# Performance work log

Hardware: AMD Instinct MI355X
Metric: run time of the kernel (lower is better)

Reference implementation:

```python
import jax, jax.numpy as jnp
import numpy as np

B, IN_CHAN, CHAN, H, W = 8, 64, 64, 56, 56


def setup_inputs() -> dict:
    key = jax.random.key(0)
    k1, k2, k3, k4 = jax.random.split(key, 4)
    x = jax.random.normal(k1, (B, IN_CHAN, H, W), dtype=jnp.float32)
    eye23 = jnp.eye(3, dtype=jnp.float32)[:2]  # [2,3] identity affine
    geoParams = eye23[None, None] + 0.1 * jax.random.normal(k2, (CHAN, IN_CHAN, 2, 3), dtype=jnp.float32)
    linComb = jax.random.uniform(k3, (CHAN, IN_CHAN), dtype=jnp.float32)
    boxParams = eye23[None] + 0.1 * jax.random.normal(k4, (CHAN, 2, 3), dtype=jnp.float32)
    return {"x": x, "geoParams": geoParams, "linComb": linComb, "boxParams": boxParams}


def _sample_coords(theta, Hs, Ws):
    # F.affine_grid with align_corners=False: base grid at pixel centers in [-1,1]
    xs = 2.0 * (jnp.arange(Ws, dtype=jnp.float32) + 0.5) / Ws - 1.0  # [W]
    ys = 2.0 * (jnp.arange(Hs, dtype=jnp.float32) + 0.5) / Hs - 1.0  # [H]
    gx = theta[..., 0, 0, None, None] * xs[None, :] + theta[..., 0, 1, None, None] * ys[:, None] + theta[..., 0, 2, None, None]
    gy = theta[..., 1, 0, None, None] * xs[None, :] + theta[..., 1, 1, None, None] * ys[:, None] + theta[..., 1, 2, None, None]
    # grid_sample unnormalize (align_corners=False)
    ix = ((gx + 1.0) * Ws - 1.0) / 2.0
    iy = ((gy + 1.0) * Hs - 1.0) / 2.0
    return ix, iy  # theta.shape[:-2] + (Hs, Ws)


def _corners(ix, iy, Hs, Ws):
    # bilinear corner flat-indices and weights (zero padding via validity mask)
    ix0 = jnp.floor(ix)
    iy0 = jnp.floor(iy)
    out = []
    for dx in (0.0, 1.0):
        for dy in (0.0, 1.0):
            cx = ix0 + dx
            cy = iy0 + dy
            w = (1.0 - jnp.abs(ix - cx)) * (1.0 - jnp.abs(iy - cy))
            valid = (cx >= 0) & (cx <= Ws - 1) & (cy >= 0) & (cy <= Hs - 1)
            idx = jnp.clip(cy, 0, Hs - 1).astype(jnp.int32) * Ws + jnp.clip(cx, 0, Ws - 1).astype(jnp.int32)
            out.append((idx, w * valid.astype(w.dtype)))
    return out


def reference(x, geoParams, linComb, boxParams):
    Bn, IC, Hs, Ws = x.shape
    C = geoParams.shape[0]
    HW = Hs * Ws
    ix, iy = _sample_coords(geoParams, Hs, Ws)  # [C, IC, H, W]
    flat = x.reshape(Bn, IC, HW)
    ic_idx = jnp.arange(IC)[None, :, None]  # broadcast with [C, IC, HW] indices
    out = jnp.zeros((Bn, C, HW), dtype=x.dtype)
    for idx, w in _corners(ix, iy, Hs, Ws):
        idxf = idx.reshape(C, IC, HW)
        wf = w.reshape(C, IC, HW)
        g = flat[:, ic_idx, idxf]  # [B, C, IC, HW] gathered corner values
        out = out + jnp.einsum('bcip,cip,ci->bcp', g, wf, linComb)
    out = out.reshape(Bn, C, Hs, Ws)
    # BoxPool: grid_sample of an all-ones image == sum of valid corner weights
    bix, biy = _sample_coords(boxParams, Hs, Ws)  # [C, H, W]
    box = jnp.zeros((C, Hs, Ws), dtype=x.dtype)
    for _, w in _corners(bix, biy, Hs, Ws):
        box = box + w
    return out * box[None]
```

## Files before the change

### kernel.cpp

```cpp
#include <hip/hip_runtime.h>

#define NB 8
#define ICN 64
#define NC 64
#define H 56
#define W 56
#define HW (H*W)
#define PH 58
#define PW 58
#define PHW (PH*PW)

typedef __attribute__((ext_vector_type(8))) _Float16 half8;

__global__ __launch_bounds__(256) void prep_kernel(
    const float* __restrict__ geo, const float* __restrict__ lin,
    float* __restrict__ prm)
{
    const int i = blockIdx.x * 256 + threadIdx.x;
    if (i >= NC * ICN) return;
    const float t00 = geo[i*6+0], t01 = geo[i*6+1], t02 = geo[i*6+2];
    const float t10 = geo[i*6+3], t11 = geo[i*6+4], t12 = geo[i*6+5];
    prm[i*8+0] = t00;
    prm[i*8+1] = t01;
    prm[i*8+2] = -27.5f*(t00+t01) + 28.f*t02 + 27.5f;
    prm[i*8+3] = t10;
    prm[i*8+4] = t11;
    prm[i*8+5] = -27.5f*(t10+t11) + 28.f*t12 + 27.5f;
    prm[i*8+6] = lin[i];
    prm[i*8+7] = 0.f;
}

__global__ __launch_bounds__(256) void transpose_pad_kernel(
    const float* __restrict__ x, _Float16* __restrict__ xt)
{
    const int id = blockIdx.x * 256 + threadIdx.x;
    if (id >= ICN * HW) return;
    const int ic = id / HW;
    const int p  = id - ic * HW;
    const int h  = p / W;
    const int w  = p - h * W;
    half8 v;
    #pragma unroll
    for (int b = 0; b < NB; ++b)
        v[b] = (_Float16)x[(size_t)b * ICN * HW + id];
    const size_t dst = ((size_t)ic * PHW + (size_t)(h + 1) * PW + (w + 1)) * NB;
    *(half8*)(xt + dst) = v;
}

__global__ __launch_bounds__(64) void geom_h_kernel(
    const _Float16* __restrict__ xt,
    const float* __restrict__ prm,
    const float* __restrict__ boxp,
    float* __restrict__ out)
{
    const int c = blockIdx.x;
    const int p = blockIdx.y * 64 + threadIdx.x;
    const int h = p / W;
    const int w = p - h * W;
    const float wf = (float)w, hf = (float)h;

    float acc[NB];
    #pragma unroll
    for (int b = 0; b < NB; ++b) acc[b] = 0.f;

    const float* pp = prm + (size_t)c * ICN * 8;

    for (int icc = 0; icc < ICN; icc += 4) {
        half8 hacc;
        #pragma unroll
        for (int b = 0; b < NB; ++b) hacc[b] = (_Float16)0.f;

        #pragma unroll
        for (int k = 0; k < 4; ++k) {
            const float* q = pp + (icc + k) * 8;
            const float ixf = fmaf(q[0], wf, fmaf(q[1], hf, q[2]));
            const float iyf = fmaf(q[3], wf, fmaf(q[4], hf, q[5]));
            const float l   = q[6];

            const float fcx0 = fminf(fmaxf(floorf(ixf), -1.f), 55.f);
            const float fcy0 = fminf(fmaxf(floorf(iyf), -1.f), 55.f);
            const float wx0 = fmaxf(0.f, 1.f - fabsf(ixf - fcx0));
            const float wx1 = fmaxf(0.f, 1.f - fabsf(ixf - fcx0 - 1.f));
            const float wy0 = fmaxf(0.f, 1.f - fabsf(iyf - fcy0));
            const float wy1 = fmaxf(0.f, 1.f - fabsf(iyf - fcy0 - 1.f));
            const float wy0l = wy0 * l, wy1l = wy1 * l;

            const _Float16 hw00 = (_Float16)(wx0 * wy0l);
            const _Float16 hw10 = (_Float16)(wx1 * wy0l);
            const _Float16 hw01 = (_Float16)(wx0 * wy1l);
            const _Float16 hw11 = (_Float16)(wx1 * wy1l);

            const int i00 = ((int)fcy0) * PW + (int)fcx0 + (PW + 1);
            const _Float16* base = xt + ((size_t)(icc + k) * PHW + i00) * NB;

            const half8 v00 = *(const half8*)(base);
            const half8 v10 = *(const half8*)(base + NB);
            const half8 v01 = *(const half8*)(base + PW * NB);
            const half8 v11 = *(const half8*)(base + (PW + 1) * NB);

            hacc += v00 * hw00 + v10 * hw10 + v01 * hw01 + v11 * hw11;
        }

        #pragma unroll
        for (int b = 0; b < NB; ++b) acc[b] += (float)hacc[b];
    }

    float box;
    {
        const float* bp = boxp + c*6;
        const float xs = 2.0f * (wf + 0.5f) / (float)W - 1.0f;
        const float ys = 2.0f * (hf + 0.5f) / (float)H - 1.0f;
        const float gx = bp[0]*xs + bp[1]*ys + bp[2];
        const float gy = bp[3]*xs + bp[4]*ys + bp[5];
        const float ixf = ((gx + 1.f)*(float)W - 1.f) * 0.5f;
        const float iyf = ((gy + 1.f)*(float)H - 1.f) * 0.5f;
        const float ix0 = floorf(ixf), iy0 = floorf(iyf);
        const float fx = ixf - ix0, fy = iyf - iy0;
        const int cx0 = (int)ix0, cy0 = (int)iy0;
        const int cx1 = cx0 + 1,  cy1 = cy0 + 1;
        const bool vx0 = (cx0 >= 0) && (cx0 < W);
        const bool vx1 = (cx1 >= 0) && (cx1 < W);
        const bool vy0 = (cy0 >= 0) && (cy0 < H);
        const bool vy1 = (cy1 >= 0) && (cy1 < H);
        box = (1.f-fx)*(1.f-fy)*((vx0 && vy0) ? 1.f : 0.f)
            + (1.f-fx)*fy     *((vx0 && vy1) ? 1.f : 0.f)
            + fx*(1.f-fy)     *((vx1 && vy0) ? 1.f : 0.f)
            + fx*fy           *((vx1 && vy1) ? 1.f : 0.f);
    }

    #pragma unroll
    for (int b = 0; b < NB; ++b)
        out[((size_t)b*NC + c)*HW + p] = acc[b] * box;
}

__global__ __launch_bounds__(256) void geom_kernel(
    const float* __restrict__ x, const float* __restrict__ geo,
    const float* __restrict__ lin, const float* __restrict__ boxp,
    float* __restrict__ out)
{
    const int c = blockIdx.x;
    const int p = blockIdx.y * blockDim.x + threadIdx.x;
    if (p >= HW) return;
    const int h = p / W;
    const int w = p - h * W;
    const float xs = 2.0f * ((float)w + 0.5f) / (float)W - 1.0f;
    const float ys = 2.0f * ((float)h + 0.5f) / (float)H - 1.0f;

    float acc[NB];
    #pragma unroll
    for (int b = 0; b < NB; ++b) acc[b] = 0.f;

    const float* gp = geo + c * ICN * 6;
    const float* lc = lin + c * ICN;

    for (int ic = 0; ic < ICN; ++ic) {
        const float t00 = gp[ic*6+0], t01 = gp[ic*6+1], t02 = gp[ic*6+2];
        const float t10 = gp[ic*6+3], t11 = gp[ic*6+4], t12 = gp[ic*6+5];
        const float l = lc[ic];
        const float gx = t00*xs + t01*ys + t02;
        const float gy = t10*xs + t11*ys + t12;
        const float ixf = ((gx + 1.f)*(float)W - 1.f) * 0.5f;
        const float iyf = ((gy + 1.f)*(float)H - 1.f) * 0.5f;
        const float ix0 = floorf(ixf), iy0 = floorf(iyf);
        const float fx = ixf - ix0, fy = iyf - iy0;
        const int cx0 = (int)ix0, cy0 = (int)iy0;
        const int cx1 = cx0 + 1,  cy1 = cy0 + 1;
        const bool vx0 = (cx0 >= 0) && (cx0 <= W-1);
        const bool vx1 = (cx1 >= 0) && (cx1 <= W-1);
        const bool vy0 = (cy0 >= 0) && (cy0 <= H-1);
        const bool vy1 = (cy1 >= 0) && (cy1 <= H-1);
        const float wx0 = 1.f - fx, wx1 = fx;
        const float wy0 = 1.f - fy, wy1 = fy;
        const float w00 = wx0*wy0 * ((vx0 && vy0) ? l : 0.f);
        const float w01 = wx0*wy1 * ((vx0 && vy1) ? l : 0.f);
        const float w10 = wx1*wy0 * ((vx1 && vy0) ? l : 0.f);
        const float w11 = wx1*wy1 * ((vx1 && vy1) ? l : 0.f);
        const int icx0 = min(max(cx0, 0), W-1);
        const int icx1 = min(max(cx1, 0), W-1);
        const int icy0 = min(max(cy0, 0), H-1);
        const int icy1 = min(max(cy1, 0), H-1);
        const int i00 = icy0*W + icx0;
        const int i01 = icy1*W + icx0;
        const int i10 = icy0*W + icx1;
        const int i11 = icy1*W + icx1;
        const float* xp = x + ic * HW;
        #pragma unroll
        for (int b = 0; b < NB; ++b) {
            const float* xb = xp + (size_t)b * ICN * HW;
            acc[b] += w00*xb[i00] + w01*xb[i01] + w10*xb[i10] + w11*xb[i11];
        }
    }

    float box;
    {
        const float* bp = boxp + c*6;
        const float gx = bp[0]*xs + bp[1]*ys + bp[2];
        const float gy = bp[3]*xs + bp[4]*ys + bp[5];
        const float ixf = ((gx + 1.f)*(float)W - 1.f) * 0.5f;
        const float iyf = ((gy + 1.f)*(float)H - 1.f) * 0.5f;
        const float ix0 = floorf(ixf), iy0 = floorf(iyf);
        const float fx = ixf - ix0, fy = iyf - iy0;
        const int cx0 = (int)ix0, cy0 = (int)iy0;
        const int cx1 = cx0 + 1,  cy1 = cy0 + 1;
        const bool vx0 = (cx0 >= 0) && (cx0 < W);
        const bool vx1 = (cx1 >= 0) && (cx1 < W);
        const bool vy0 = (cy0 >= 0) && (cy0 < H);
        const bool vy1 = (cy1 >= 0) && (cy1 < H);
        box = (1.f-fx)*(1.f-fy)*((vx0 && vy0) ? 1.f : 0.f)
            + (1.f-fx)*fy     *((vx0 && vy1) ? 1.f : 0.f)
            + fx*(1.f-fy)     *((vx1 && vy0) ? 1.f : 0.f)
            + fx*fy           *((vx1 && vy1) ? 1.f : 0.f);
    }
    #pragma unroll
    for (int b = 0; b < NB; ++b)
        out[((size_t)b*NC + c)*HW + p] = acc[b] * box;
}

extern "C" void kernel_launch(void* const* d_in, const int* in_sizes, int n_in,
                              void* d_out, int out_size, void* d_ws, size_t ws_size,
                              hipStream_t stream) {
    const float* x    = (const float*)d_in[0];
    const float* geo  = (const float*)d_in[1];
    const float* lin  = (const float*)d_in[2];
    const float* boxp = (const float*)d_in[3];
    float* out = (float*)d_out;

    const size_t xt_bytes  = (size_t)ICN * PHW * NB * sizeof(_Float16);
    const size_t prm_off   = (xt_bytes + 255) & ~(size_t)255;
    const size_t prm_bytes = (size_t)NC * ICN * 8 * sizeof(float);
    if (ws_size >= prm_off + prm_bytes) {
        _Float16* xt = (_Float16*)d_ws;
        float* prm = (float*)((char*)d_ws + prm_off);
        hipMemsetAsync(d_ws, 0, xt_bytes, stream);
        hipLaunchKernelGGL(prep_kernel, dim3((NC*ICN + 255)/256), dim3(256),
                           0, stream, geo, lin, prm);
        hipLaunchKernelGGL(transpose_pad_kernel, dim3((ICN*HW + 255)/256), dim3(256),
                           0, stream, x, xt);
        hipLaunchKernelGGL(geom_h_kernel, dim3(NC, 49), dim3(64),
                           0, stream, xt, prm, boxp, out);
    } else {
        hipLaunchKernelGGL(geom_kernel, dim3(NC, (HW + 255)/256), dim3(256),
                           0, stream, x, geo, lin, boxp, out);
    }
}
```

Before: 55.01 us.

## Merge setup kernels, drop memset, split input channels across two waves

Combines the parameter prep and the transpose/pad into one setup kernel that also writes the zero padding itself, so the separate memset and one launch are no longer needed. The main kernel now uses 128 threads per block. Each of two wavefronts handles half of the input channels, and the partial sums are reduced through shared memory before the box scaling and store. This doubles the wave count to hide gather latency, at the cost of a barrier and some idle time for the second wave at the end.

```diff
diff --git a/kernel.cpp b/kernel.cpp
--- a/kernel.cpp
+++ b/kernel.cpp
@@ -12,49 +12,55 @@
 
 typedef __attribute__((ext_vector_type(8))) _Float16 half8;
 
-__global__ __launch_bounds__(256) void prep_kernel(
-    const float* __restrict__ geo, const float* __restrict__ lin,
-    float* __restrict__ prm)
+__global__ __launch_bounds__(256) void setup_kernel(
+    const float* __restrict__ x, const float* __restrict__ geo,
+    const float* __restrict__ lin,
+    _Float16* __restrict__ xt, float* __restrict__ prm)
 {
-    const int i = blockIdx.x * 256 + threadIdx.x;
-    if (i >= NC * ICN) return;
-    const float t00 = geo[i*6+0], t01 = geo[i*6+1], t02 = geo[i*6+2];
-    const float t10 = geo[i*6+3], t11 = geo[i*6+4], t12 = geo[i*6+5];
-    prm[i*8+0] = t00;
-    prm[i*8+1] = t01;
-    prm[i*8+2] = -27.5f*(t00+t01) + 28.f*t02 + 27.5f;
-    prm[i*8+3] = t10;
-    prm[i*8+4] = t11;
-    prm[i*8+5] = -27.5f*(t10+t11) + 28.f*t12 + 27.5f;
-    prm[i*8+6] = lin[i];
-    prm[i*8+7] = 0.f;
-}
-
-__global__ __launch_bounds__(256) void transpose_pad_kernel(
-    const float* __restrict__ x, _Float16* __restrict__ xt)
-{
-    const int id = blockIdx.x * 256 + threadIdx.x;
-    if (id >= ICN * HW) return;
-    const int ic = id / HW;
-    const int p  = id - ic * HW;
-    const int h  = p / W;
-    const int w  = p - h * W;
-    half8 v;
-    #pragma unroll
-    for (int b = 0; b < NB; ++b)
-        v[b] = (_Float16)x[(size_t)b * ICN * HW + id];
-    const size_t dst = ((size_t)ic * PHW + (size_t)(h + 1) * PW + (w + 1)) * NB;
-    *(half8*)(xt + dst) = v;
-}
-
-__global__ __launch_bounds__(64) void geom_h_kernel(
+    const int bx = blockIdx.x;
+    if (bx < 64) {
+        const int i = bx * 256 + threadIdx.x;
+        const float t00 = geo[i*6+0], t01 = geo[i*6+1], t02 = geo[i*6+2];
+        const float t10 = geo[i*6+3], t11 = geo[i*6+4], t12 = geo[i*6+5];
+        prm[i*8+0] = t00;
+        prm[i*8+1] = t01;
+        prm[i*8+2] = -27.5f*(t00+t01) + 28.f*t02 + 27.5f;
+        prm[i*8+3] = t10;
+        prm[i*8+4] = t11;
+        prm[i*8+5] = -27.5f*(t10+t11) + 28.f*t12 + 27.5f;
+        prm[i*8+6] = lin[i];
+        prm[i*8+7] = 0.f;
+    } else {
+        const int id = (bx - 64) * 256 + threadIdx.x;
+        const int ic  = id / PHW;
+        const int rem = id - ic * PHW;
+        const int ph  = rem / PW;
+        const int pw  = rem - ph * PW;
+        half8 v;
+        #pragma unroll
+        for (int b = 0; b < NB; ++b) v[b] = (_Float16)0.f;
+        if (ph >= 1 && ph <= H && pw >= 1 && pw <= W) {
+            const int p = (ph - 1) * W + (pw - 1);
+            #pragma unroll
+            for (int b = 0; b < NB; ++b)
+                v[b] = (_Float16)x[(size_t)b * ICN * HW + ic * HW + p];
+        }
+        *(half8*)(xt + (size_t)id * NB) = v;
+    }
+}
+
+__global__ __launch_bounds__(128) void geom_h2_kernel(
     const _Float16* __restrict__ xt,
     const float* __restrict__ prm,
     const float* __restrict__ boxp,
     float* __restrict__ out)
 {
-    const int c = blockIdx.x;
-    const int p = blockIdx.y * 64 + threadIdx.x;
+    __shared__ float lds[64][NB + 1];
+
+    const int c    = blockIdx.x;
+    const int lane = threadIdx.x & 63;
+    const int wv   = threadIdx.x >> 6;
+    const int p    = blockIdx.y * 64 + lane;
     const int h = p / W;
     const int w = p - h * W;
     const float wf = (float)w, hf = (float)h;
@@ -63,9 +69,10 @@
     #pragma unroll
     for (int b = 0; b < NB; ++b) acc[b] = 0.f;
 
-    const float* pp = prm + (size_t)c * ICN * 8;
-
-    for (int icc = 0; icc < ICN; icc += 4) {
+    const float* pp = prm + ((size_t)c * ICN + wv * 32) * 8;
+    const int ic0 = wv * 32;
+
+    for (int icc = 0; icc < 32; icc += 4) {
         half8 hacc;
         #pragma unroll
         for (int b = 0; b < NB; ++b) hacc[b] = (_Float16)0.f;
@@ -91,7 +98,7 @@
             const _Float16 hw11 = (_Float16)(wx1 * wy1l);
 
             const int i00 = ((int)fcy0) * PW + (int)fcx0 + (PW + 1);
-            const _Float16* base = xt + ((size_t)(icc + k) * PHW + i00) * NB;
+            const _Float16* base = xt + ((size_t)(ic0 + icc + k) * PHW + i00) * NB;
 
             const half8 v00 = *(const half8*)(base);
             const half8 v10 = *(const half8*)(base + NB);
@@ -105,32 +112,42 @@
         for (int b = 0; b < NB; ++b) acc[b] += (float)hacc[b];
     }
 
-    float box;
-    {
-        const float* bp = boxp + c*6;
-        const float xs = 2.0f * (wf + 0.5f) / (float)W - 1.0f;
-        const float ys = 2.0f * (hf + 0.5f) / (float)H - 1.0f;
-        const float gx = bp[0]*xs + bp[1]*ys + bp[2];
-        const float gy = bp[3]*xs + bp[4]*ys + bp[5];
-        const float ixf = ((gx + 1.f)*(float)W - 1.f) * 0.5f;
-        const float iyf = ((gy + 1.f)*(float)H - 1.f) * 0.5f;
-        const float ix0 = floorf(ixf), iy0 = floorf(iyf);
-        const float fx = ixf - ix0, fy = iyf - iy0;
-        const int cx0 = (int)ix0, cy0 = (int)iy0;
-        const int cx1 = cx0 + 1,  cy1 = cy0 + 1;
-        const bool vx0 = (cx0 >= 0) && (cx0 < W);
-        const bool vx1 = (cx1 >= 0) && (cx1 < W);
-        const bool vy0 = (cy0 >= 0) && (cy0 < H);
-        const bool vy1 = (cy1 >= 0) && (cy1 < H);
-        box = (1.f-fx)*(1.f-fy)*((vx0 && vy0) ? 1.f : 0.f)
-            + (1.f-fx)*fy     *((vx0 && vy1) ? 1.f : 0.f)
-            + fx*(1.f-fy)     *((vx1 && vy0) ? 1.f : 0.f)
-            + fx*fy           *((vx1 && vy1) ? 1.f : 0.f);
-    }
-
-    #pragma unroll
-    for (int b = 0; b < NB; ++b)
-        out[((size_t)b*NC + c)*HW + p] = acc[b] * box;
+    if (wv == 1) {
+        #pragma unroll
+        for (int b = 0; b < NB; ++b) lds[lane][b] = acc[b];
+    }
+    __syncthreads();
+    if (wv == 0) {
+        #pragma unroll
+        for (int b = 0; b < NB; ++b) acc[b] += lds[lane][b];
+
+        float box;
+        {
+            const float* bp = boxp + c*6;
+            const float xs = 2.0f * (wf + 0.5f) / (float)W - 1.0f;
+            const float ys = 2.0f * (hf + 0.5f) / (float)H - 1.0f;
+            const float gx = bp[0]*xs + bp[1]*ys + bp[2];
+            const float gy = bp[3]*xs + bp[4]*ys + bp[5];
+            const float ixf = ((gx + 1.f)*(float)W - 1.f) * 0.5f;
+            const float iyf = ((gy + 1.f)*(float)H - 1.f) * 0.5f;
+            const float ix0 = floorf(ixf), iy0 = floorf(iyf);
+            const float fx = ixf - ix0, fy = iyf - iy0;
+            const int cx0 = (int)ix0, cy0 = (int)iy0;
+            const int cx1 = cx0 + 1,  cy1 = cy0 + 1;
+            const bool vx0 = (cx0 >= 0) && (cx0 < W);
+            const bool vx1 = (cx1 >= 0) && (cx1 < W);
+            const bool vy0 = (cy0 >= 0) && (cy0 < H);
+            const bool vy1 = (cy1 >= 0) && (cy1 < H);
+            box = (1.f-fx)*(1.f-fy)*((vx0 && vy0) ? 1.f : 0.f)
+                + (1.f-fx)*fy     *((vx0 && vy1) ? 1.f : 0.f)
+                + fx*(1.f-fy)     *((vx1 && vy0) ? 1.f : 0.f)
+                + fx*fy           *((vx1 && vy1) ? 1.f : 0.f);
+        }
+
+        #pragma unroll
+        for (int b = 0; b < NB; ++b)
+            out[((size_t)b*NC + c)*HW + p] = acc[b] * box;
+    }
 }
 
 __global__ __launch_bounds__(256) void geom_kernel(
@@ -231,12 +248,9 @@
     if (ws_size >= prm_off + prm_bytes) {
         _Float16* xt = (_Float16*)d_ws;
         float* prm = (float*)((char*)d_ws + prm_off);
-        hipMemsetAsync(d_ws, 0, xt_bytes, stream);
-        hipLaunchKernelGGL(prep_kernel, dim3((NC*ICN + 255)/256), dim3(256),
-                           0, stream, geo, lin, prm);
-        hipLaunchKernelGGL(transpose_pad_kernel, dim3((ICN*HW + 255)/256), dim3(256),
-                           0, stream, x, xt);
-        hipLaunchKernelGGL(geom_h_kernel, dim3(NC, 49), dim3(64),
+        hipLaunchKernelGGL(setup_kernel, dim3(64 + (ICN*PHW)/256), dim3(256),
+                           0, stream, x, geo, lin, xt, prm);
+        hipLaunchKernelGGL(geom_h2_kernel, dim3(NC, 49), dim3(128),
                            0, stream, xt, prm, boxp, out);
     } else {
         hipLaunchKernelGGL(geom_kernel, dim3(NC, (HW + 255)/256), dim3(256),
```

After: 55.82 us. No clear change (+1.5%).
